# Kernel optimization log

Hardware: AMD Instinct MI355X
Metric: run time of the kernel (lower is better)

## Reference

```python
import jax, jax.numpy as jnp
import numpy as np

BITS = 4
PACK = 32 // BITS  # 8 nibbles per int32
GROUPSIZE = 128
MASK = (1 << BITS) - 1


def dequantize(qweight, qzeros, scales):
    """GPTQ dequant: W[i,o] = scales[g[i],o] * (q[i,o] - (z[g[i],o] + 1))."""
    shifts = (jnp.arange(PACK, dtype=jnp.int32) * BITS)
    # qweight: [in/8, out] packed along input dim -> [in, out]
    wq = (qweight[:, None, :] >> shifts[None, :, None]) & MASK
    wq = wq.reshape(-1, qweight.shape[1])  # [in, out] int32 in [0,15]
    # qzeros: [G, out/8] packed along output dim -> [G, out]
    zq = ((qzeros[:, :, None] >> shifts[None, None, :]) & MASK) + 1
    zq = zq.reshape(qzeros.shape[0], -1)  # [G, out]
    g_idx = jnp.arange(wq.shape[0], dtype=jnp.int32) // GROUPSIZE  # [in]
    # fp16 dequant like the CUDA/Triton GPTQ kernels
    W = (wq - zq[g_idx]).astype(jnp.float16) * scales[g_idx]
    return W  # [in, out] fp16


def setup_inputs() -> dict:
    key = jax.random.key(0)
    kx, kw, kz, ks, kb = jax.random.split(key, 5)
    in_f, out_f, groups = 4096, 4096, 4096 // GROUPSIZE
    x = jax.random.normal(kx, (8192, in_f), dtype=jnp.float16)
    qweight = jax.random.randint(kw, (in_f // PACK, out_f), 0, 2147483647, dtype=jnp.int32)
    qzeros = jax.random.randint(kz, (groups, out_f // PACK), 0, 2147483647, dtype=jnp.int32)
    scales = (jax.random.uniform(ks, (groups, out_f), dtype=jnp.float32) * 0.01 + 0.001).astype(jnp.float16)
    bias = jax.random.normal(kb, (out_f,), dtype=jnp.float16)
    return {"x": x, "qweight": qweight, "qzeros": qzeros, "scales": scales, "bias": bias}


def reference(x, qweight, qzeros, scales, bias):
    W = dequantize(qweight, qzeros, scales)  # [in, out] fp16
    # accumulate in fp32, output fp16 (matches CaiGPTQLinearOp fp16 output)
    out = jnp.matmul(x, W, preferred_element_type=jnp.float32).astype(jnp.float16)
    out = out + bias
    return out
```

## Files before the change

kernel.cpp:

```cpp
#include <hip/hip_runtime.h>

typedef _Float16 half8 __attribute__((ext_vector_type(8)));
typedef _Float16 half2v __attribute__((ext_vector_type(2)));
typedef float floatx4 __attribute__((ext_vector_type(4)));

#define K_IN 4096
#define N_OUT 4096
#define NGROUPS 32
#define BM 128
#define BN 128
#define LDA 40

__device__ __forceinline__ unsigned int pkcvt(float lo, float hi) {
    return __builtin_bit_cast(unsigned int, __builtin_amdgcn_cvt_pkrtz(lo, hi));
}

__global__ __launch_bounds__(256)
void cvt_x_f16(const float* __restrict__ x, _Float16* __restrict__ x16) {
    const size_t idx = ((size_t)blockIdx.x * 256 + threadIdx.x) * 8;
    const float4 a = *(const float4*)(x + idx);
    const float4 b = *(const float4*)(x + idx + 4);
    uint4 u;
    u.x = pkcvt(a.x, a.y);  u.y = pkcvt(a.z, a.w);
    u.z = pkcvt(b.x, b.y);  u.w = pkcvt(b.z, b.w);
    *(uint4*)(x16 + idx) = u;
}

__global__ __launch_bounds__(256)
void dequant_wt(const int* __restrict__ qweight,
                const int* __restrict__ qzeros,
                const float* __restrict__ scales,
                _Float16* __restrict__ wt)
{
    const int tid = threadIdx.x;
    const int col = blockIdx.x * 64 + (tid & 63);
    const int g   = blockIdx.y;
    const int i   = tid >> 6;

    const unsigned int zw = (unsigned int)qzeros[g * (N_OUT / 8) + (col >> 3)];
    const unsigned int z  = (zw >> ((col & 7) * 4)) & 0xFu;
    const unsigned int cb = 0x6400u + z + 1u;
    const half2v c2 = __builtin_bit_cast(half2v, cb | (cb << 16));
    const float  s  = scales[g * N_OUT + col];
    const half2v s2 = __builtin_bit_cast(half2v, pkcvt(s, s));

    const int kc0 = g * 16 + i * 4;
#pragma unroll
    for (int r = 0; r < 4; ++r) {
        const unsigned int q = (unsigned int)qweight[(size_t)(kc0 + r) * N_OUT + col];
        const unsigned int r0 = (q & 0x000F000Fu)         | 0x64006400u;
        const unsigned int r1 = ((q >> 4) & 0x000F000Fu)  | 0x64006400u;
        const unsigned int r2 = ((q >> 8) & 0x000F000Fu)  | 0x64006400u;
        const unsigned int r3 = ((q >> 12) & 0x000F000Fu) | 0x64006400u;
        unsigned int p0 = __builtin_bit_cast(unsigned int,
                          (half2v)((__builtin_bit_cast(half2v, r0) - c2) * s2));
        unsigned int p1 = __builtin_bit_cast(unsigned int,
                          (half2v)((__builtin_bit_cast(half2v, r1) - c2) * s2));
        unsigned int p2 = __builtin_bit_cast(unsigned int,
                          (half2v)((__builtin_bit_cast(half2v, r2) - c2) * s2));
        unsigned int p3 = __builtin_bit_cast(unsigned int,
                          (half2v)((__builtin_bit_cast(half2v, r3) - c2) * s2));
        uint4 nat;
        nat.x = (p0 & 0xFFFFu) | (p1 << 16);
        nat.y = (p2 & 0xFFFFu) | (p3 << 16);
        nat.z = (p0 >> 16) | (p1 & 0xFFFF0000u);
        nat.w = (p2 >> 16) | (p3 & 0xFFFF0000u);
        *(uint4*)(wt + (size_t)col * K_IN + (kc0 + r) * 8) = nat;
    }
}

__global__ __launch_bounds__(256, 3)
void gemm_f16(const _Float16* __restrict__ x16,
              const _Float16* __restrict__ wt,
              const float* __restrict__ bias,
              float* __restrict__ out)
{
    __shared__ alignas(16) _Float16 As[2][BM * LDA];

    const int tid  = threadIdx.x;
    const int lane = tid & 63;
    const int wave = tid >> 6;
    const int l15  = lane & 15;
    const int l4   = lane >> 4;

    const int blockN = blockIdx.x * BN;
    const int blockM = blockIdx.y * BM;

    floatx4 acc[8][2] = {};

    const int srow = tid >> 2;
    const int sch  = tid & 3;
    const _Float16* xr0 = x16 + (size_t)(blockM + srow) * K_IN + sch * 8;
    const _Float16* xr1 = xr0 + (size_t)64 * K_IN;
    _Float16* lw0 = &As[0][srow * LDA + sch * 8];
    _Float16* lw1 = &As[0][(srow + 64) * LDA + sch * 8];

    int ncol[2];
    const _Float16* wp[2];
#pragma unroll
    for (int j = 0; j < 2; ++j) {
        ncol[j] = blockN + wave * 32 + j * 16 + l15;
        wp[j]   = wt + (size_t)ncol[j] * K_IN + l4 * 8;
    }

    uint4 pa = *(const uint4*)(const void*)xr0;
    uint4 pb = *(const uint4*)(const void*)xr1;
    uint4 pw0 = *(const uint4*)(const void*)wp[0];
    uint4 pw1 = *(const uint4*)(const void*)wp[1];

    for (int t = 0; t < 4 * NGROUPS; ++t) {
        const int buf = t & 1;

        *(uint4*)(void*)(lw0 + buf * (BM * LDA)) = pa;
        *(uint4*)(void*)(lw1 + buf * (BM * LDA)) = pb;

        half8 bfrag[2];
        bfrag[0] = __builtin_bit_cast(half8, pw0);
        bfrag[1] = __builtin_bit_cast(half8, pw1);

        const int t1 = (t + 1 < 4 * NGROUPS) ? t + 1 : t;
        pa  = *(const uint4*)(const void*)(xr0 + t1 * 32);
        pb  = *(const uint4*)(const void*)(xr1 + t1 * 32);
        pw0 = *(const uint4*)(const void*)(wp[0] + t1 * 32);
        pw1 = *(const uint4*)(const void*)(wp[1] + t1 * 32);

        __syncthreads();

        half8 afrag[8];
#pragma unroll
        for (int i = 0; i < 8; ++i)
            afrag[i] = *(const half8*)(const void*)
                &As[buf][(i * 16 + l15) * LDA + l4 * 8];

#pragma unroll
        for (int i = 0; i < 8; ++i) {
            acc[i][0] = __builtin_amdgcn_mfma_f32_16x16x32_f16(
                afrag[i], bfrag[0], acc[i][0], 0, 0, 0);
            acc[i][1] = __builtin_amdgcn_mfma_f32_16x16x32_f16(
                afrag[i], bfrag[1], acc[i][1], 0, 0, 0);
        }
    }

#pragma unroll
    for (int j = 0; j < 2; ++j) {
        const int n = ncol[j];
        const float bv = bias[n];
#pragma unroll
        for (int i = 0; i < 8; ++i) {
            const int m = blockM + i * 16 + l4 * 4;
#pragma unroll
            for (int r = 0; r < 4; ++r)
                out[(size_t)(m + r) * N_OUT + n] = acc[i][j][r] + bv;
        }
    }
}

__global__ __launch_bounds__(256, 2)
void gptq_gemm_fused(const float* __restrict__ x,
                     const int*   __restrict__ qweight,
                     const int*   __restrict__ qzeros,
                     const float* __restrict__ scales,
                     const float* __restrict__ bias,
                     float*       __restrict__ out)
{
    __shared__ alignas(16) _Float16 As[2][BM * LDA];

    const int tid  = threadIdx.x;
    const int lane = tid & 63;
    const int wave = tid >> 6;
    const int l15  = lane & 15;
    const int l4   = lane >> 4;

    const int blockN = blockIdx.x * BN;
    const int blockM = blockIdx.y * BM;

    floatx4 acc[8][2] = {};

    const int srow = tid >> 2;
    const int sch  = tid & 3;
    const float* xr0 = x + (size_t)(blockM + srow) * K_IN + sch * 8;
    const float* xr1 = xr0 + (size_t)64 * K_IN;
    _Float16* lw0 = &As[0][srow * LDA + sch * 8];
    _Float16* lw1 = &As[0][(srow + 64) * LDA + sch * 8];

    int ncol[2];
#pragma unroll
    for (int j = 0; j < 2; ++j) ncol[j] = blockN + wave * 32 + j * 16 + l15;

    unsigned int zraw[2]; float sraw[2];
#pragma unroll
    for (int j = 0; j < 2; ++j) {
        zraw[j] = (unsigned int)qzeros[ncol[j] >> 3];
        sraw[j] = scales[ncol[j]];
    }
    float4 pa0 = *(const float4*)(xr0);
    float4 pa1 = *(const float4*)(xr0 + 4);
    float4 pb0 = *(const float4*)(xr1);
    float4 pb1 = *(const float4*)(xr1 + 4);
    unsigned int pq[2];
    {
        const int* qr = qweight + (size_t)l4 * N_OUT;
#pragma unroll
        for (int j = 0; j < 2; ++j) pq[j] = (unsigned int)qr[ncol[j]];
    }

    for (int g = 0; g < NGROUPS; ++g) {
        unsigned int c2u[2], s2u[2];
#pragma unroll
        for (int j = 0; j < 2; ++j) {
            const unsigned int z  = (zraw[j] >> ((ncol[j] & 7) * 4)) & 0xFu;
            const unsigned int cb = 0x6400u + z + 1u;
            c2u[j] = cb | (cb << 16);
            s2u[j] = pkcvt(sraw[j], sraw[j]);
        }
        const int gn = (g + 1 < NGROUPS) ? g + 1 : g;
#pragma unroll
        for (int j = 0; j < 2; ++j) {
            zraw[j] = (unsigned int)qzeros[gn * (N_OUT / 8) + (ncol[j] >> 3)];
            sraw[j] = scales[gn * N_OUT + ncol[j]];
        }

#pragma unroll
        for (int kk = 0; kk < 4; ++kk) {
            const int t   = g * 4 + kk;
            const int buf = t & 1;

            uint4 ra, rb;
            ra.x = pkcvt(pa0.x, pa1.x);  ra.y = pkcvt(pa0.y, pa1.y);
            ra.z = pkcvt(pa0.z, pa1.z);  ra.w = pkcvt(pa0.w, pa1.w);
            rb.x = pkcvt(pb0.x, pb1.x);  rb.y = pkcvt(pb0.y, pb1.y);
            rb.z = pkcvt(pb0.z, pb1.z);  rb.w = pkcvt(pb0.w, pb1.w);
            *(uint4*)(void*)(lw0 + buf * (BM * LDA)) = ra;
            *(uint4*)(void*)(lw1 + buf * (BM * LDA)) = rb;

            unsigned int bq[2] = {pq[0], pq[1]};

            const int t1 = (t + 1 < 4 * NGROUPS) ? t + 1 : t;
            pa0 = *(const float4*)(xr0 + t1 * 32);
            pa1 = *(const float4*)(xr0 + t1 * 32 + 4);
            pb0 = *(const float4*)(xr1 + t1 * 32);
            pb1 = *(const float4*)(xr1 + t1 * 32 + 4);
            {
                const int* qr = qweight + (size_t)(t1 * 4 + l4) * N_OUT;
#pragma unroll
                for (int j = 0; j < 2; ++j) pq[j] = (unsigned int)qr[ncol[j]];
            }

            __syncthreads();

            half8 bfrag[2];
#pragma unroll
            for (int j = 0; j < 2; ++j) {
                const unsigned int q = bq[j];
                const unsigned int r0 = (q & 0x000F000Fu)        | 0x64006400u;
                const unsigned int r1 = ((q >> 4) & 0x000F000Fu) | 0x64006400u;
                const unsigned int r2 = ((q >> 8) & 0x000F000Fu) | 0x64006400u;
                const unsigned int r3 = ((q >> 12) & 0x000F000Fu)| 0x64006400u;
                const half2v c2 = __builtin_bit_cast(half2v, c2u[j]);
                const half2v s2 = __builtin_bit_cast(half2v, s2u[j]);
                union { unsigned int u[4]; half8 h; } pk;
                pk.u[0] = __builtin_bit_cast(unsigned int,
                          (half2v)((__builtin_bit_cast(half2v, r0) - c2) * s2));
                pk.u[1] = __builtin_bit_cast(unsigned int,
                          (half2v)((__builtin_bit_cast(half2v, r1) - c2) * s2));
                pk.u[2] = __builtin_bit_cast(unsigned int,
                          (half2v)((__builtin_bit_cast(half2v, r2) - c2) * s2));
                pk.u[3] = __builtin_bit_cast(unsigned int,
                          (half2v)((__builtin_bit_cast(half2v, r3) - c2) * s2));
                bfrag[j] = pk.h;
            }

            half8 afrag[8];
#pragma unroll
            for (int i = 0; i < 8; ++i)
                afrag[i] = *(const half8*)(const void*)
                    &As[buf][(i * 16 + l15) * LDA + l4 * 8];

#pragma unroll
            for (int i = 0; i < 8; ++i)
#pragma unroll
                for (int j = 0; j < 2; ++j)
                    acc[i][j] = __builtin_amdgcn_mfma_f32_16x16x32_f16(
                        afrag[i], bfrag[j], acc[i][j], 0, 0, 0);
        }
    }

#pragma unroll
    for (int j = 0; j < 2; ++j) {
        const int n = ncol[j];
        const float bv = bias[n];
#pragma unroll
        for (int i = 0; i < 8; ++i) {
            const int m = blockM + i * 16 + l4 * 4;
#pragma unroll
            for (int r = 0; r < 4; ++r)
                out[(size_t)(m + r) * N_OUT + n] = acc[i][j][r] + bv;
        }
    }
}

extern "C" void kernel_launch(void* const* d_in, const int* in_sizes, int n_in,
                              void* d_out, int out_size, void* d_ws, size_t ws_size,
                              hipStream_t stream) {
    const float* x    = (const float*)d_in[0];
    const int*   qw   = (const int*)d_in[1];
    const int*   qz   = (const int*)d_in[2];
    const float* sc   = (const float*)d_in[3];
    const float* bias = (const float*)d_in[4];
    float*       out  = (float*)d_out;

    const int M = in_sizes[0] / K_IN;

    const size_t x16_bytes = (size_t)M * K_IN * sizeof(_Float16);
    const size_t wt_bytes  = (size_t)N_OUT * K_IN * sizeof(_Float16);

    if (ws_size >= x16_bytes + wt_bytes) {
        _Float16* x16 = (_Float16*)d_ws;
        _Float16* wtp = (_Float16*)((char*)d_ws + x16_bytes);

        cvt_x_f16<<<(int)((size_t)M * K_IN / 2048), 256, 0, stream>>>(x, x16);
        dequant_wt<<<dim3(N_OUT / 64, NGROUPS), 256, 0, stream>>>(qw, qz, sc, wtp);
        gemm_f16<<<dim3(N_OUT / BN, M / BM), 256, 0, stream>>>(x16, wtp, bias, out);
    } else {
        gptq_gemm_fused<<<dim3(N_OUT / BN, M / BM), 256, 0, stream>>>(
            x, qw, qz, sc, bias, out);
    }
}
```

Measured before the change: 569.5 us.

## Use 2x2 wave tiling, XOR-swizzled LDS, and XCD-aware block remapping in GEMM

The GEMM kernel now arranges its four waves as a 2x2 grid of 64x64 subtiles instead of 1x4 strips of 32 columns. Each wave loads 4 A fragments and 4 B fragments rather than 8 A and 2 B, which cuts LDS reads per MFMA. The padded LDS row stride is replaced by an unpadded 32-half row with an XOR swizzle to avoid bank conflicts. Block indices are remapped so consecutive blocks on each XCD share N columns and M rows, aiming for better L2 locality. The trade-offs are more direct global B loads per thread and a remap that hardcodes the grid shape.

```diff
diff --git a/kernel.cpp b/kernel.cpp
--- a/kernel.cpp
+++ b/kernel.cpp
@@ -9,7 +9,6 @@
 #define NGROUPS 32
 #define BM 128
 #define BN 128
-#define LDA 40
 
 __device__ __forceinline__ unsigned int pkcvt(float lo, float hi) {
     return __builtin_bit_cast(unsigned int, __builtin_amdgcn_cvt_pkrtz(lo, hi));
@@ -75,79 +74,89 @@
               const float* __restrict__ bias,
               float* __restrict__ out)
 {
-    __shared__ alignas(16) _Float16 As[2][BM * LDA];
+    __shared__ alignas(16) _Float16 As[2][BM * 32];
 
     const int tid  = threadIdx.x;
     const int lane = tid & 63;
     const int wave = tid >> 6;
+    const int wm   = wave >> 1;
+    const int wn   = wave & 1;
     const int l15  = lane & 15;
     const int l4   = lane >> 4;
 
-    const int blockN = blockIdx.x * BN;
-    const int blockM = blockIdx.y * BM;
-
-    floatx4 acc[8][2] = {};
+    const int lin   = blockIdx.y * gridDim.x + blockIdx.x;
+    const int xcd   = lin & 7;
+    const int idx   = lin >> 3;
+    const int phase = idx >> 7;
+    const int blockN = (xcd * 4 + phase * 2 + (idx & 1)) * BN;
+    const int blockM = ((idx >> 1) & 63) * BM;
+
+    floatx4 acc[4][4] = {};
 
     const int srow = tid >> 2;
     const int sch  = tid & 3;
+    const int schw = sch ^ ((srow >> 1) & 3);
     const _Float16* xr0 = x16 + (size_t)(blockM + srow) * K_IN + sch * 8;
     const _Float16* xr1 = xr0 + (size_t)64 * K_IN;
-    _Float16* lw0 = &As[0][srow * LDA + sch * 8];
-    _Float16* lw1 = &As[0][(srow + 64) * LDA + sch * 8];
-
-    int ncol[2];
-    const _Float16* wp[2];
-#pragma unroll
-    for (int j = 0; j < 2; ++j) {
-        ncol[j] = blockN + wave * 32 + j * 16 + l15;
+    _Float16* lw0 = &As[0][srow * 32 + schw * 8];
+    _Float16* lw1 = lw0 + 64 * 32;
+
+    int ncol[4];
+    const _Float16* wp[4];
+#pragma unroll
+    for (int j = 0; j < 4; ++j) {
+        ncol[j] = blockN + wn * 64 + j * 16 + l15;
         wp[j]   = wt + (size_t)ncol[j] * K_IN + l4 * 8;
     }
+
+    const int rswz = (l15 >> 1) & 3;
 
     uint4 pa = *(const uint4*)(const void*)xr0;
     uint4 pb = *(const uint4*)(const void*)xr1;
-    uint4 pw0 = *(const uint4*)(const void*)wp[0];
-    uint4 pw1 = *(const uint4*)(const void*)wp[1];
+    uint4 pw[4];
+#pragma unroll
+    for (int j = 0; j < 4; ++j) pw[j] = *(const uint4*)(const void*)wp[j];
 
     for (int t = 0; t < 4 * NGROUPS; ++t) {
         const int buf = t & 1;
 
-        *(uint4*)(void*)(lw0 + buf * (BM * LDA)) = pa;
-        *(uint4*)(void*)(lw1 + buf * (BM * LDA)) = pb;
-
-        half8 bfrag[2];
-        bfrag[0] = __builtin_bit_cast(half8, pw0);
-        bfrag[1] = __builtin_bit_cast(half8, pw1);
+        *(uint4*)(void*)(lw0 + buf * (BM * 32)) = pa;
+        *(uint4*)(void*)(lw1 + buf * (BM * 32)) = pb;
+
+        half8 bfrag[4];
+#pragma unroll
+        for (int j = 0; j < 4; ++j) bfrag[j] = __builtin_bit_cast(half8, pw[j]);
 
         const int t1 = (t + 1 < 4 * NGROUPS) ? t + 1 : t;
-        pa  = *(const uint4*)(const void*)(xr0 + t1 * 32);
-        pb  = *(const uint4*)(const void*)(xr1 + t1 * 32);
-        pw0 = *(const uint4*)(const void*)(wp[0] + t1 * 32);
-        pw1 = *(const uint4*)(const void*)(wp[1] + t1 * 32);
+        pa = *(const uint4*)(const void*)(xr0 + t1 * 32);
+        pb = *(const uint4*)(const void*)(xr1 + t1 * 32);
+#pragma unroll
+        for (int j = 0; j < 4; ++j)
+            pw[j] = *(const uint4*)(const void*)(wp[j] + t1 * 32);
 
         __syncthreads();
 
-        half8 afrag[8];
-#pragma unroll
-        for (int i = 0; i < 8; ++i)
+        half8 afrag[4];
+#pragma unroll
+        for (int i = 0; i < 4; ++i)
             afrag[i] = *(const half8*)(const void*)
-                &As[buf][(i * 16 + l15) * LDA + l4 * 8];
-
-#pragma unroll
-        for (int i = 0; i < 8; ++i) {
-            acc[i][0] = __builtin_amdgcn_mfma_f32_16x16x32_f16(
-                afrag[i], bfrag[0], acc[i][0], 0, 0, 0);
-            acc[i][1] = __builtin_amdgcn_mfma_f32_16x16x32_f16(
-                afrag[i], bfrag[1], acc[i][1], 0, 0, 0);
-        }
-    }
-
-#pragma unroll
-    for (int j = 0; j < 2; ++j) {
+                &As[buf][(wm * 64 + i * 16 + l15) * 32 + (l4 ^ rswz) * 8];
+
+#pragma unroll
+        for (int i = 0; i < 4; ++i)
+#pragma unroll
+            for (int j = 0; j < 4; ++j)
+                acc[i][j] = __builtin_amdgcn_mfma_f32_16x16x32_f16(
+                    afrag[i], bfrag[j], acc[i][j], 0, 0, 0);
+    }
+
+#pragma unroll
+    for (int j = 0; j < 4; ++j) {
         const int n = ncol[j];
         const float bv = bias[n];
 #pragma unroll
-        for (int i = 0; i < 8; ++i) {
-            const int m = blockM + i * 16 + l4 * 4;
+        for (int i = 0; i < 4; ++i) {
+            const int m = blockM + wm * 64 + i * 16 + l4 * 4;
 #pragma unroll
             for (int r = 0; r < 4; ++r)
                 out[(size_t)(m + r) * N_OUT + n] = acc[i][j][r] + bv;
@@ -163,7 +172,8 @@
                      const float* __restrict__ bias,
                      float*       __restrict__ out)
 {
-    __shared__ alignas(16) _Float16 As[2][BM * LDA];
+#define LDA 40
+    __shared__ alignas(16) _Float16 Asf[2][BM * LDA];
 
     const int tid  = threadIdx.x;
     const int lane = tid & 63;
@@ -180,8 +190,8 @@
     const int sch  = tid & 3;
     const float* xr0 = x + (size_t)(blockM + srow) * K_IN + sch * 8;
     const float* xr1 = xr0 + (size_t)64 * K_IN;
-    _Float16* lw0 = &As[0][srow * LDA + sch * 8];
-    _Float16* lw1 = &As[0][(srow + 64) * LDA + sch * 8];
+    _Float16* lw0 = &Asf[0][srow * LDA + sch * 8];
+    _Float16* lw1 = &Asf[0][(srow + 64) * LDA + sch * 8];
 
     int ncol[2];
 #pragma unroll
@@ -274,7 +284,7 @@
 #pragma unroll
             for (int i = 0; i < 8; ++i)
                 afrag[i] = *(const half8*)(const void*)
-                    &As[buf][(i * 16 + l15) * LDA + l4 * 8];
+                    &Asf[buf][(i * 16 + l15) * LDA + l4 * 8];
 
 #pragma unroll
             for (int i = 0; i < 8; ++i)
@@ -297,6 +307,7 @@
                 out[(size_t)(m + r) * N_OUT + n] = acc[i][j][r] + bv;
         }
     }
+#undef LDA
 }
 
 extern "C" void kernel_launch(void* const* d_in, const int* in_sizes, int n_in,
```

Result: slower. 764.9 us (+34.3%).

## Load A tiles directly to LDS with global_load_lds and XOR-swizzled layout

Applied to the files above, without the earlier changes.

In the fp16 GEMM kernel, A-tile staging through registers is replaced by direct global-to-LDS loads (global_load_lds, 16 bytes per lane). Because that path cannot use a padded layout, the LDS tile becomes unpadded with an XOR swizzle on the chunk index to avoid bank conflicts. Synchronisation changes from __syncthreads to an explicit vmcnt wait plus s_barrier, and the next tile is prefetched after the fragment reads. This saves VGPRs and store instructions, but it depends on correct hand-written waitcnt ordering and on the swizzle matching between writers and readers.

```diff
diff --git a/kernel.cpp b/kernel.cpp
--- a/kernel.cpp
+++ b/kernel.cpp
@@ -9,10 +9,15 @@
 #define NGROUPS 32
 #define BM 128
 #define BN 128
-#define LDA 40
 
 __device__ __forceinline__ unsigned int pkcvt(float lo, float hi) {
     return __builtin_bit_cast(unsigned int, __builtin_amdgcn_cvt_pkrtz(lo, hi));
+}
+
+__device__ __forceinline__ void gll16(const _Float16* g, _Float16* l) {
+    __builtin_amdgcn_global_load_lds(
+        (const __attribute__((address_space(1))) void*)g,
+        (__attribute__((address_space(3))) void*)l, 16, 0, 0);
 }
 
 __global__ __launch_bounds__(256)
@@ -75,7 +80,7 @@
               const float* __restrict__ bias,
               float* __restrict__ out)
 {
-    __shared__ alignas(16) _Float16 As[2][BM * LDA];
+    __shared__ alignas(16) _Float16 As[2 * BM * 32];
 
     const int tid  = threadIdx.x;
     const int lane = tid & 63;
@@ -88,56 +93,59 @@
 
     floatx4 acc[8][2] = {};
 
-    const int srow = tid >> 2;
-    const int sch  = tid & 3;
-    const _Float16* xr0 = x16 + (size_t)(blockM + srow) * K_IN + sch * 8;
-    const _Float16* xr1 = xr0 + (size_t)64 * K_IN;
-    _Float16* lw0 = &As[0][srow * LDA + sch * 8];
-    _Float16* lw1 = &As[0][(srow + 64) * LDA + sch * 8];
+    const int grow  = wave * 32 + (lane >> 2);
+    const int gchnk = (lane & 3) ^ ((lane >> 3) & 3);
+    const _Float16* gsrc0 = x16 + (size_t)(blockM + grow) * K_IN + gchnk * 8;
+    const _Float16* gsrc1 = gsrc0 + (size_t)16 * K_IN;
+    _Float16* ldst0 = &As[wave * 1024];
+    _Float16* ldst1 = ldst0 + 512;
+
+    const int rdoff = (l4 ^ ((l15 >> 1) & 3)) * 8;
 
     int ncol[2];
-    const _Float16* wp[2];
-#pragma unroll
-    for (int j = 0; j < 2; ++j) {
-        ncol[j] = blockN + wave * 32 + j * 16 + l15;
-        wp[j]   = wt + (size_t)ncol[j] * K_IN + l4 * 8;
-    }
-
-    uint4 pa = *(const uint4*)(const void*)xr0;
-    uint4 pb = *(const uint4*)(const void*)xr1;
-    uint4 pw0 = *(const uint4*)(const void*)wp[0];
-    uint4 pw1 = *(const uint4*)(const void*)wp[1];
+    const _Float16* wp0;
+    const _Float16* wp1;
+    ncol[0] = blockN + wave * 32 + l15;
+    ncol[1] = ncol[0] + 16;
+    wp0 = wt + (size_t)ncol[0] * K_IN + l4 * 8;
+    wp1 = wt + (size_t)ncol[1] * K_IN + l4 * 8;
+
+    gll16(gsrc0, ldst0);
+    gll16(gsrc1, ldst1);
+    __builtin_amdgcn_sched_barrier(0);
+    uint4 pw0 = *(const uint4*)(const void*)wp0;
+    uint4 pw1 = *(const uint4*)(const void*)wp1;
 
     for (int t = 0; t < 4 * NGROUPS; ++t) {
         const int buf = t & 1;
 
-        *(uint4*)(void*)(lw0 + buf * (BM * LDA)) = pa;
-        *(uint4*)(void*)(lw1 + buf * (BM * LDA)) = pb;
-
-        half8 bfrag[2];
-        bfrag[0] = __builtin_bit_cast(half8, pw0);
-        bfrag[1] = __builtin_bit_cast(half8, pw1);
-
-        const int t1 = (t + 1 < 4 * NGROUPS) ? t + 1 : t;
-        pa  = *(const uint4*)(const void*)(xr0 + t1 * 32);
-        pb  = *(const uint4*)(const void*)(xr1 + t1 * 32);
-        pw0 = *(const uint4*)(const void*)(wp[0] + t1 * 32);
-        pw1 = *(const uint4*)(const void*)(wp[1] + t1 * 32);
-
-        __syncthreads();
+        asm volatile("s_waitcnt vmcnt(2)" ::: "memory");
+        __builtin_amdgcn_s_barrier();
+        asm volatile("" ::: "memory");
 
         half8 afrag[8];
 #pragma unroll
         for (int i = 0; i < 8; ++i)
             afrag[i] = *(const half8*)(const void*)
-                &As[buf][(i * 16 + l15) * LDA + l4 * 8];
+                &As[buf * 4096 + (i * 16 + l15) * 32 + rdoff];
+
+        half8 b0 = __builtin_bit_cast(half8, pw0);
+        half8 b1 = __builtin_bit_cast(half8, pw1);
+
+        const int t1 = (t + 1 < 4 * NGROUPS) ? t + 1 : t;
+        const int bn = buf ^ 1;
+        gll16(gsrc0 + t1 * 32, ldst0 + bn * 4096);
+        gll16(gsrc1 + t1 * 32, ldst1 + bn * 4096);
+        __builtin_amdgcn_sched_barrier(0);
+        pw0 = *(const uint4*)(const void*)(wp0 + t1 * 32);
+        pw1 = *(const uint4*)(const void*)(wp1 + t1 * 32);
 
 #pragma unroll
         for (int i = 0; i < 8; ++i) {
             acc[i][0] = __builtin_amdgcn_mfma_f32_16x16x32_f16(
-                afrag[i], bfrag[0], acc[i][0], 0, 0, 0);
+                afrag[i], b0, acc[i][0], 0, 0, 0);
             acc[i][1] = __builtin_amdgcn_mfma_f32_16x16x32_f16(
-                afrag[i], bfrag[1], acc[i][1], 0, 0, 0);
+                afrag[i], b1, acc[i][1], 0, 0, 0);
         }
     }
 
@@ -163,7 +171,8 @@
                      const float* __restrict__ bias,
                      float*       __restrict__ out)
 {
-    __shared__ alignas(16) _Float16 As[2][BM * LDA];
+#define LDA 40
+    __shared__ alignas(16) _Float16 Asf[2][BM * LDA];
 
     const int tid  = threadIdx.x;
     const int lane = tid & 63;
@@ -180,8 +189,8 @@
     const int sch  = tid & 3;
     const float* xr0 = x + (size_t)(blockM + srow) * K_IN + sch * 8;
     const float* xr1 = xr0 + (size_t)64 * K_IN;
-    _Float16* lw0 = &As[0][srow * LDA + sch * 8];
-    _Float16* lw1 = &As[0][(srow + 64) * LDA + sch * 8];
+    _Float16* lw0 = &Asf[0][srow * LDA + sch * 8];
+    _Float16* lw1 = &Asf[0][(srow + 64) * LDA + sch * 8];
 
     int ncol[2];
 #pragma unroll
@@ -274,7 +283,7 @@
 #pragma unroll
             for (int i = 0; i < 8; ++i)
                 afrag[i] = *(const half8*)(const void*)
-                    &As[buf][(i * 16 + l15) * LDA + l4 * 8];
+                    &Asf[buf][(i * 16 + l15) * LDA + l4 * 8];
 
 #pragma unroll
             for (int i = 0; i < 8; ++i)
@@ -297,6 +306,7 @@
                 out[(size_t)(m + r) * N_OUT + n] = acc[i][j][r] + bv;
         }
     }
+#undef LDA
 }
 
 extern "C" void kernel_launch(void* const* d_in, const int* in_sizes, int n_in,
```

Result: no change. 560.3 us (-1.6%).
